# Performance work log

Hardware: AMD Instinct MI355X
Metric: run time of the kernel (lower is better)

Reference implementation:

```python
import jax, jax.numpy as jnp
import numpy as np

D = 1024
H = 16
HD = D // H
B = 2
T = 2048


def _rope_tables(t, hd):
    inv_freq = 1.0 / (10000.0 ** (np.arange(0, hd, 2, dtype=np.float32) / hd))
    ang = np.arange(t, dtype=np.float32)[:, None] * inv_freq[None, :]  # [T, hd/2]
    emb = np.concatenate([ang, ang], axis=-1)  # [T, hd]
    return jnp.asarray(np.cos(emb)), jnp.asarray(np.sin(emb))


def setup_inputs() -> dict:
    key = jax.random.key(0)
    kx, kq, kk, kv, ko = jax.random.split(key, 5)
    scale = 0.02
    x = jax.random.normal(kx, (B, T, D), dtype=jnp.float32)
    cos, sin = _rope_tables(T, HD)
    mask = jnp.tril(jnp.ones((T, T), dtype=jnp.int32))[None, None]  # [1,1,T,T]
    wq = jax.random.normal(kq, (D, D), dtype=jnp.float32) * scale
    wk = jax.random.normal(kk, (D, D), dtype=jnp.float32) * scale
    wv = jax.random.normal(kv, (D, D), dtype=jnp.float32) * scale
    wo = jax.random.normal(ko, (D, D), dtype=jnp.float32) * scale
    return {"x": x, "cos": cos, "sin": sin, "mask": mask,
            "wq": wq, "wk": wk, "wv": wv, "wo": wo}


def _rotate_half(t):
    t1, t2 = jnp.split(t, 2, axis=-1)
    return jnp.concatenate((-t2, t1), axis=-1)


def reference(x, cos, sin, mask, wq, wk, wv, wo):
    Bx, Tx, C = x.shape
    hd = C // H
    # nn.Linear: y = x @ W.T  -> [B,T,H,hd] -> [B,H,T,hd]
    q = (x @ wq.T).reshape(Bx, Tx, H, hd).transpose(0, 2, 1, 3)
    k = (x @ wk.T).reshape(Bx, Tx, H, hd).transpose(0, 2, 1, 3)
    v = (x @ wv.T).reshape(Bx, Tx, H, hd).transpose(0, 2, 1, 3)
    c = cos[:Tx][None, None]  # [1,1,T,hd]
    s = sin[:Tx][None, None]
    q = q * c + _rotate_half(q) * s
    k = k * c + _rotate_half(k) * s
    att = jnp.einsum('bhqd,bhkd->bhqk', q, k) * (hd ** -0.5)
    att = jnp.where(mask[:, :, :Tx, :Tx] == 0, -jnp.inf, att)
    att = jax.nn.softmax(att, axis=-1)
    out = jnp.einsum('bhqk,bhkd->bhqd', att, v)
    out = out.transpose(0, 2, 1, 3).reshape(Bx, Tx, C)
    return out @ wo.T
```

## Files before the change

kernel.cpp:

```cpp
#include <hip/hip_runtime.h>
#include <math.h>

constexpr int D  = 1024;
constexpr int H  = 16;
constexpr int HD = 64;
constexpr int B  = 2;
constexpr int T  = 2048;
constexpr int M  = B * T;

constexpr size_t XSZ = (size_t)M * D;
constexpr size_t WSZ = (size_t)D * D;

typedef float  f32x4   __attribute__((ext_vector_type(4)));
typedef float  f32x16  __attribute__((ext_vector_type(16)));
typedef __bf16 bf16x8  __attribute__((ext_vector_type(8)));
typedef __bf16 bf16x4  __attribute__((ext_vector_type(4)));
typedef unsigned u32x2 __attribute__((ext_vector_type(2)));
typedef unsigned u32x4 __attribute__((ext_vector_type(4)));

static __device__ inline f32x4 mfma16(bf16x8 a, bf16x8 b, f32x4 c) {
  return __builtin_amdgcn_mfma_f32_16x16x32_bf16(a, b, c, 0, 0, 0);
}
static __device__ inline f32x16 mfma32(bf16x8 a, bf16x8 b, f32x16 c) {
  return __builtin_amdgcn_mfma_f32_32x32x16_bf16(a, b, c, 0, 0, 0);
}
static __device__ inline unsigned cvtpk(float a, float b) {
  unsigned r;
  asm("v_cvt_pk_bf16_f32 %0, %1, %2" : "=v"(r) : "v"(a), "v"(b));
  return r;
}
static __device__ inline u32x2 plswap(unsigned a, unsigned b) {
  return __builtin_amdgcn_permlane32_swap(a, b, false, false);
}
static __device__ inline void gload16(const __bf16* g, __bf16* l) {
  __builtin_amdgcn_global_load_lds(
      (const __attribute__((address_space(1))) void*)g,
      (__attribute__((address_space(3))) void*)l, 16, 0, 0);
}

__global__ __launch_bounds__(256)
void cvt_all(const float* __restrict__ x, const float* __restrict__ wq,
             const float* __restrict__ wk, const float* __restrict__ wv,
             const float* __restrict__ wo, __bf16* __restrict__ out) {
  size_t idx = ((size_t)blockIdx.x * 256 + threadIdx.x) * 8;
  const float* src;
  if      (idx < XSZ)            src = x  + idx;
  else if (idx < XSZ + WSZ)      src = wq + (idx - XSZ);
  else if (idx < XSZ + 2 * WSZ)  src = wk + (idx - XSZ - WSZ);
  else if (idx < XSZ + 3 * WSZ)  src = wv + (idx - XSZ - 2 * WSZ);
  else                           src = wo + (idx - XSZ - 3 * WSZ);
  float4 a = *reinterpret_cast<const float4*>(src);
  float4 b = *reinterpret_cast<const float4*>(src + 4);
  bf16x8 o;
  o[0] = (__bf16)a.x; o[1] = (__bf16)a.y; o[2] = (__bf16)a.z; o[3] = (__bf16)a.w;
  o[4] = (__bf16)b.x; o[5] = (__bf16)b.y; o[6] = (__bf16)b.z; o[7] = (__bf16)b.w;
  *reinterpret_cast<bf16x8*>(out + idx) = o;
}

template<int MODE>
__global__ __launch_bounds__(256)
void gemm_mfma(const __bf16* __restrict__ A,
               const __bf16* __restrict__ W0, const __bf16* __restrict__ W1,
               const __bf16* __restrict__ W2,
               const float* __restrict__ cosT, const float* __restrict__ sinT,
               void* __restrict__ out0, void* __restrict__ out1,
               void* __restrict__ out2) {
  constexpr int BM  = (MODE == 0) ? 64 : 128;
  constexpr int NMT = BM / 32;
  __shared__ __bf16 As[BM * 64];
  __shared__ __bf16 Bs[128 * 64];

  const int tid  = threadIdx.x;
  const int lane = tid & 63;
  const int w    = tid >> 6;
  const int wm   = w >> 1;
  const int wn   = w & 1;
  const int l15  = lane & 15, lg = lane >> 4;
  const int m0   = blockIdx.y * BM;

  int which, n0;
  const __bf16* Bw;
  if (MODE == 1) {
    which = blockIdx.x >> 3;
    n0 = (blockIdx.x & 7) * 128;
    Bw = which == 0 ? W0 : which == 1 ? W1 : W2;
  } else {
    which = 0;
    n0 = blockIdx.x * 128;
    Bw = W0;
  }

  f32x4 acc[NMT][4];
  #pragma unroll
  for (int i = 0; i < NMT; ++i)
    #pragma unroll
    for (int j = 0; j < 4; ++j) acc[i][j] = (f32x4){0.f, 0.f, 0.f, 0.f};

  const int r0 = tid >> 3;
  const int c0 = (tid & 7) * 8;

  for (int k0 = 0; k0 < 1024; k0 += 64) {
    #pragma unroll
    for (int i = 0; i < BM / 32; ++i)
      gload16(A + (size_t)(m0 + r0 + 32 * i) * 1024 + k0 + c0,
              As + (tid + 256 * i) * 8);
    #pragma unroll
    for (int i = 0; i < 4; ++i)
      gload16(Bw + (size_t)(n0 + r0 + 32 * i) * 1024 + k0 + c0,
              Bs + (tid + 256 * i) * 8);
    __syncthreads();

    #pragma unroll
    for (int ks = 0; ks < 2; ++ks) {
      bf16x8 af[NMT], bfr[4];
      #pragma unroll
      for (int mt = 0; mt < NMT; ++mt)
        af[mt] = *reinterpret_cast<const bf16x8*>(
            &As[(wm * (BM / 2) + mt * 16 + l15) * 64 + ks * 32 + lg * 8]);
      #pragma unroll
      for (int nt = 0; nt < 4; ++nt)
        bfr[nt] = *reinterpret_cast<const bf16x8*>(
            &Bs[(wn * 64 + nt * 16 + l15) * 64 + ks * 32 + lg * 8]);
      #pragma unroll
      for (int mt = 0; mt < NMT; ++mt)
        #pragma unroll
        for (int nt = 0; nt < 4; ++nt)
          acc[mt][nt] = mfma16(af[mt], bfr[nt], acc[mt][nt]);
    }
    __syncthreads();
  }

  if (MODE == 0) {
    float* o = (float*)out0;
    #pragma unroll
    for (int mt = 0; mt < NMT; ++mt) {
      const int mb = m0 + wm * (BM / 2) + mt * 16 + lg * 4;
      #pragma unroll
      for (int nt = 0; nt < 4; ++nt) {
        const int n = n0 + wn * 64 + nt * 16 + l15;
        #pragma unroll
        for (int r = 0; r < 4; ++r)
          o[(size_t)(mb + r) * 1024 + n] = acc[mt][nt][r];
      }
    }
  } else if (which < 2) {
    __bf16* dst = which == 0 ? (__bf16*)out0 : (__bf16*)out1;
    const float qs = (which == 0) ? 0.180336880f : 1.0f;
    const int h = (n0 + wn * 64) >> 6;
    const int e  = l15 & 7;
    const int Lh = (l15 >> 3) << 5;
    #pragma unroll
    for (int mt = 0; mt < NMT; ++mt) {
      const int tb   = m0 + wm * (BM / 2) + mt * 16 + lg * 4;
      const int bb   = tb >> 11;
      const int tloc = tb & 2047;
      const int bh   = bb * H + h;
      #pragma unroll
      for (int r = 0; r < 4; ++r) {
        const int t = tloc + r;
        const int L = (t & 31) + Lh;
        size_t fb;
        if (which == 0)
          fb = ((size_t)bh * 64 + (t >> 5)) * 4;
        else
          fb = (((size_t)bh * 32 + (t >> 6)) * 2 + ((t >> 5) & 1)) * 4;
        #pragma unroll
        for (int nt = 0; nt < 2; ++nt) {
          const int hd = nt * 16 + l15;
          const float c = cosT[t * HD + hd];
          const float s = sinT[t * HD + hd];
          const float v1 = acc[mt][nt][r];
          const float v2 = acc[mt][nt + 2][r];
          dst[(fb + nt)     * 512 + L * 8 + e] = (__bf16)((v1 * c - v2 * s) * qs);
          dst[(fb + nt + 2) * 512 + L * 8 + e] = (__bf16)((v2 * c + v1 * s) * qs);
        }
      }
    }
  } else {
    __bf16* dst = (__bf16*)out2;
    const int h = (n0 + wn * 64) >> 6;
    #pragma unroll
    for (int mt = 0; mt < NMT; ++mt) {
      const int tb   = m0 + wm * (BM / 2) + mt * 16 + lg * 4;
      const int bb   = tb >> 11;
      const int tloc = tb & 2047;
      const int bh   = bb * H + h;
      const int jt   = tloc >> 6;
      const int kt   = tloc & 63;
      const int Lk   = ((kt >> 3) & 1) << 5;
      const int e0   = kt & 7;
      const size_t fb = (((size_t)bh * 32 + jt) * 2) * 4 + (kt >> 4);
      #pragma unroll
      for (int nt = 0; nt < 4; ++nt) {
        const int hd = nt * 16 + l15;
        const int dg = hd >> 5;
        const int L  = (hd & 31) + Lk;
        bf16x4 ov;
        #pragma unroll
        for (int r = 0; r < 4; ++r) ov[r] = (__bf16)acc[mt][nt][r];
        *reinterpret_cast<bf16x4*>(
            &dst[(fb + (size_t)dg * 4) * 512 + L * 8 + e0]) = ov;
      }
    }
  }
}

__global__ __launch_bounds__(256, 2)
void attn_v14(const __bf16* __restrict__ Qf, const __bf16* __restrict__ Kf,
              const __bf16* __restrict__ Vf, __bf16* __restrict__ Ob) {
  const int tid  = threadIdx.x;
  const int lane = tid & 63;
  const int w    = tid >> 6;
  const int l31  = lane & 31;
  const int hi   = lane >> 5;
  const int bx   = blockIdx.x;
  const int by   = blockIdx.y;
  const int bh   = (bx & 7) + 8 * (by >> 3);
  const int x    = (bx >> 3) + 2 * (by & 7);

  const int wi = (bh < 16) ? w : (w ^ 1);
  const int qt = (wi == 0) ? 2 * x : (wi == 1) ? 63 - 2 * x
               : (wi == 2) ? 2 * x + 1 : 62 - 2 * x;
  const int q0w = qt * 32;
  const int NT  = (qt >> 1) + 1;

  const __bf16* qbase = Qf + (((size_t)bh * 64 + qt) * 4) * 512 + lane * 8;
  bf16x8 qfr[4];
  #pragma unroll
  for (int st = 0; st < 4; ++st)
    qfr[st] = *reinterpret_cast<const bf16x8*>(qbase + st * 512);

  f32x16 zv;
  #pragma unroll
  for (int i = 0; i < 16; ++i) zv[i] = 0.f;

  float m_run = -INFINITY, l_run = 0.f;
  f32x16 oacc0, oacc1;
  #pragma unroll
  for (int i = 0; i < 16; ++i) { oacc0[i] = 0.f; oacc1[i] = 0.f; }

  const __bf16* kbase = Kf + ((size_t)bh * 32 * 8) * 512 + lane * 8;
  const __bf16* vbase = Vf + ((size_t)bh * 32 * 8) * 512 + lane * 8;

#define LOADK8(K0, K1, K2, K3, K4, K5, K6, K7, jj)                            \
  do {                                                                        \
    const __bf16* _kp = kbase + (size_t)(jj) * 8 * 512;                       \
    K0 = *reinterpret_cast<const bf16x8*>(_kp);                               \
    K1 = *reinterpret_cast<const bf16x8*>(_kp + 512);                         \
    K2 = *reinterpret_cast<const bf16x8*>(_kp + 1024);                        \
    K3 = *reinterpret_cast<const bf16x8*>(_kp + 1536);                        \
    K4 = *reinterpret_cast<const bf16x8*>(_kp + 2048);                        \
    K5 = *reinterpret_cast<const bf16x8*>(_kp + 2560);                        \
    K6 = *reinterpret_cast<const bf16x8*>(_kp + 3072);                        \
    K7 = *reinterpret_cast<const bf16x8*>(_kp + 3584);                        \
    __builtin_amdgcn_sched_barrier(0);        \
  } while (0)

#define TILE64(K0, K1, K2, K3, K4, K5, K6, K7, jj)                            \
  do {                                                                        \
            \
    const __bf16* _vp = vbase + (size_t)(jj) * 8 * 512;                       \
    bf16x8 Va00 = *reinterpret_cast<const bf16x8*>(_vp);                      \
    bf16x8 Va01 = *reinterpret_cast<const bf16x8*>(_vp + 512);                \
    bf16x8 Vb00 = *reinterpret_cast<const bf16x8*>(_vp + 1024);               \
    bf16x8 Vb01 = *reinterpret_cast<const bf16x8*>(_vp + 1536);               \
    bf16x8 Va10 = *reinterpret_cast<const bf16x8*>(_vp + 2048);               \
    bf16x8 Va11 = *reinterpret_cast<const bf16x8*>(_vp + 2560);               \
    bf16x8 Vb10 = *reinterpret_cast<const bf16x8*>(_vp + 3072);               \
    bf16x8 Vb11 = *reinterpret_cast<const bf16x8*>(_vp + 3584);               \
    __builtin_amdgcn_sched_barrier(0);                                        \
               \
    f32x16 s0a = mfma32(K0, qfr[0], zv);                                      \
    f32x16 s0b = mfma32(K1, qfr[1], zv);                                      \
    f32x16 s1a = mfma32(K4, qfr[0], zv);                                      \
    f32x16 s1b = mfma32(K5, qfr[1], zv);                                      \
    s0a = mfma32(K2, qfr[2], s0a);                                            \
    s0b = mfma32(K3, qfr[3], s0b);                                            \
    s1a = mfma32(K6, qfr[2], s1a);                                            \
    s1b = mfma32(K7, qfr[3], s1b);                                            \
    f32x16 sv0, sv1;                                                          \
    _Pragma("unroll")                                                         \
    for (int _i = 0; _i < 16; ++_i) {                                         \
      sv0[_i] = s0a[_i] + s0b[_i];                                            \
      sv1[_i] = s1a[_i] + s1b[_i];                                            \
    }                                                                         \
    if ((jj) == NT - 1) {         \
      const int _q  = q0w + l31;                                              \
      const int _k0 = (jj) * 64 + 4 * hi;                                     \
      _Pragma("unroll")                                                       \
      for (int _r = 0; _r < 16; ++_r) {                                       \
        const int _key = _k0 + (_r & 3) + 8 * (_r >> 2);                      \
        if (_key > _q)      sv0[_r] = -INFINITY;                              \
        if (_key + 32 > _q) sv1[_r] = -INFINITY;                              \
      }                                                                       \
    }                                                                         \
                                             \
    float _mx[16];                                                            \
    _Pragma("unroll")                                                         \
    for (int _i = 0; _i < 16; ++_i) _mx[_i] = fmaxf(sv0[_i], sv1[_i]);        \
    _Pragma("unroll")                                                         \
    for (int _s = 8; _s > 0; _s >>= 1)                                        \
      _Pragma("unroll")                                                       \
      for (int _i = 0; _i < 8; ++_i)                                          \
        if (_i < _s) _mx[_i] = fmaxf(_mx[_i], _mx[_i + _s]);                  \
    union { float f; unsigned u; } _cv; _cv.f = _mx[0];                       \
    u32x2 _sw = plswap(_cv.u, _cv.u);                                         \
    union { unsigned u; float f; } _c0, _c1; _c0.u = _sw[0]; _c1.u = _sw[1];  \
    const float _pmax = fmaxf(_c0.f, _c1.f);                                  \
    if (__any(_pmax > m_run + 8.f)) {                                         \
      const float _mn = fmaxf(m_run, _pmax);                                  \
      const float _rs = exp2f(m_run - _mn);                                   \
      l_run *= _rs;                                                           \
      _Pragma("unroll")                                                       \
      for (int _i = 0; _i < 16; ++_i) { oacc0[_i] *= _rs; oacc1[_i] *= _rs; } \
      m_run = _mn;                                                            \
    }                                                                         \
    _Pragma("unroll")                                                         \
    for (int _i = 0; _i < 16; ++_i) {                                         \
      sv0[_i] = exp2f(sv0[_i] - m_run);                                       \
      sv1[_i] = exp2f(sv1[_i] - m_run);                                       \
    }                                                                         \
    float _sm[16];                                                            \
    _Pragma("unroll")                                                         \
    for (int _i = 0; _i < 16; ++_i) _sm[_i] = sv0[_i] + sv1[_i];              \
    _Pragma("unroll")                                                         \
    for (int _s = 8; _s > 0; _s >>= 1)                                        \
      _Pragma("unroll")                                                       \
      for (int _i = 0; _i < 8; ++_i)                                          \
        if (_i < _s) _sm[_i] += _sm[_i + _s];                                 \
    l_run += _sm[0];                                                          \
    unsigned _cp0[8], _cp1[8];                                                \
    _Pragma("unroll")                                                         \
    for (int _m = 0; _m < 4; ++_m) {                                          \
      _cp0[2 * _m]     = cvtpk(sv0[4 * _m],     sv0[4 * _m + 1]);             \
      _cp0[2 * _m + 1] = cvtpk(sv0[4 * _m + 2], sv0[4 * _m + 3]);             \
      _cp1[2 * _m]     = cvtpk(sv1[4 * _m],     sv1[4 * _m + 1]);             \
      _cp1[2 * _m + 1] = cvtpk(sv1[4 * _m + 2], sv1[4 * _m + 3]);             \
    }                                                                         \
    {                                                                         \
      u32x2 _r0 = plswap(_cp0[0], _cp0[2]);                                   \
      u32x2 _r1 = plswap(_cp0[1], _cp0[3]);                                   \
      union { u32x4 u; bf16x8 v; } _pu;                                       \
      _pu.u = (u32x4){_r0[0], _r1[0], _r0[1], _r1[1]};                        \
      oacc0 = mfma32(Va00, _pu.v, oacc0);                                     \
      oacc1 = mfma32(Va10, _pu.v, oacc1);                                     \
    }                                                                         \
    {                                                                         \
      u32x2 _r0 = plswap(_cp0[4], _cp0[6]);                                   \
      u32x2 _r1 = plswap(_cp0[5], _cp0[7]);                                   \
      union { u32x4 u; bf16x8 v; } _pu;                                       \
      _pu.u = (u32x4){_r0[0], _r1[0], _r0[1], _r1[1]};                        \
      oacc0 = mfma32(Va01, _pu.v, oacc0);                                     \
      oacc1 = mfma32(Va11, _pu.v, oacc1);                                     \
    }                                                                         \
    {                                                                         \
      u32x2 _r0 = plswap(_cp1[0], _cp1[2]);                                   \
      u32x2 _r1 = plswap(_cp1[1], _cp1[3]);                                   \
      union { u32x4 u; bf16x8 v; } _pu;                                       \
      _pu.u = (u32x4){_r0[0], _r1[0], _r0[1], _r1[1]};                        \
      oacc0 = mfma32(Vb00, _pu.v, oacc0);                                     \
      oacc1 = mfma32(Vb10, _pu.v, oacc1);                                     \
    }                                                                         \
    {                                                                         \
      u32x2 _r0 = plswap(_cp1[4], _cp1[6]);                                   \
      u32x2 _r1 = plswap(_cp1[5], _cp1[7]);                                   \
      union { u32x4 u; bf16x8 v; } _pu;                                       \
      _pu.u = (u32x4){_r0[0], _r1[0], _r0[1], _r1[1]};                        \
      oacc0 = mfma32(Vb01, _pu.v, oacc0);                                     \
      oacc1 = mfma32(Vb11, _pu.v, oacc1);                                     \
    }                                                                         \
  } while (0)

  bf16x8 kA0, kA1, kA2, kA3, kA4, kA5, kA6, kA7;
  bf16x8 kB0, kB1, kB2, kB3, kB4, kB5, kB6, kB7;

  LOADK8(kA0, kA1, kA2, kA3, kA4, kA5, kA6, kA7, 0);
  int j = 0;
  #pragma unroll 1
  for (;;) {
    if (j + 1 < NT) LOADK8(kB0, kB1, kB2, kB3, kB4, kB5, kB6, kB7, j + 1);
    TILE64(kA0, kA1, kA2, kA3, kA4, kA5, kA6, kA7, j);
    if (++j >= NT) break;
    if (j + 1 < NT) LOADK8(kA0, kA1, kA2, kA3, kA4, kA5, kA6, kA7, j + 1);
    TILE64(kB0, kB1, kB2, kB3, kB4, kB5, kB6, kB7, j);
    if (++j >= NT) break;
  }
#undef TILE64
#undef LOADK8

  const float l_tot = l_run + __shfl_xor(l_run, 32);
  const float inv = 1.f / l_tot;
  const int b = bh >> 4, h = bh & 15;
  const int q_abs = q0w + l31;
  const size_t rowbase = ((size_t)(b * T + q_abs)) * 1024 + h * 64;
  #pragma unroll
  for (int rg = 0; rg < 4; ++rg) {
    bf16x4 o0, o1;
    #pragma unroll
    for (int r = 0; r < 4; ++r) {
      o0[r] = (__bf16)(oacc0[rg * 4 + r] * inv);
      o1[r] = (__bf16)(oacc1[rg * 4 + r] * inv);
    }
    *reinterpret_cast<bf16x4*>(&Ob[rowbase + rg * 8 + hi * 4])      = o0;
    *reinterpret_cast<bf16x4*>(&Ob[rowbase + 32 + rg * 8 + hi * 4]) = o1;
  }
}

extern "C" void kernel_launch(void* const* d_in, const int* in_sizes, int n_in,
                              void* d_out, int out_size, void* d_ws, size_t ws_size,
                              hipStream_t stream) {
  const float* x    = (const float*)d_in[0];
  const float* cosT = (const float*)d_in[1];
  const float* sinT = (const float*)d_in[2];
  const float* wq   = (const float*)d_in[4];
  const float* wk   = (const float*)d_in[5];
  const float* wv   = (const float*)d_in[6];
  const float* wo   = (const float*)d_in[7];
  float* out = (float*)d_out;

  __bf16* xb   = (__bf16*)d_ws;
  __bf16* wqb  = xb  + XSZ;
  __bf16* wkb  = wqb + WSZ;
  __bf16* wvb  = wkb + WSZ;
  __bf16* wob  = wvb + WSZ;
  __bf16* Qfb  = wob + WSZ;
  __bf16* Kfb  = Qfb + XSZ;
  __bf16* Vfb  = Kfb + XSZ;
  __bf16* attb = Vfb + XSZ;

  cvt_all<<<(XSZ + 4 * WSZ) / 8 / 256, 256, 0, stream>>>(x, wq, wk, wv, wo, xb);

  gemm_mfma<1><<<dim3(24, 32), 256, 0, stream>>>(
      xb, wqb, wkb, wvb, cosT, sinT, Qfb, Kfb, Vfb);

  attn_v14<<<dim3(16, 32), 256, 0, stream>>>(Qfb, Kfb, Vfb, attb);

  gemm_mfma<0><<<dim3(8, 64), 256, 0, stream>>>(
      attb, wob, nullptr, nullptr, nullptr, nullptr, out, nullptr, nullptr);
}
```

Measured before the change: 143.5 us.

## Software-pipeline QK^T one tile ahead of softmax and PV in attention

Splits the attention inner tile into separate QK, softmax+PV, and V-load stages, then computes the next tile's QK^T MFMAs before the current tile's softmax so matrix work overlaps the VALU-heavy softmax. K loads are prefetched two tiles ahead. The QK accumulation also changes from two parallel partial sums to one serial chain. This raises register pressure (extra score accumulators) under the 2-waves launch bound, with a risk of spills or lower occupancy.

```diff
diff --git a/kernel.cpp b/kernel.cpp
--- a/kernel.cpp
+++ b/kernel.cpp
@@ -206,7 +206,7 @@
 }
 
 __global__ __launch_bounds__(256, 2)
-void attn_v14(const __bf16* __restrict__ Qf, const __bf16* __restrict__ Kf,
+void attn_v15(const __bf16* __restrict__ Qf, const __bf16* __restrict__ Kf,
               const __bf16* __restrict__ Vf, __bf16* __restrict__ Ob) {
   const int tid  = threadIdx.x;
   const int lane = tid & 63;
@@ -253,51 +253,50 @@
     K5 = *reinterpret_cast<const bf16x8*>(_kp + 2560);                        \
     K6 = *reinterpret_cast<const bf16x8*>(_kp + 3072);                        \
     K7 = *reinterpret_cast<const bf16x8*>(_kp + 3584);                        \
-    __builtin_amdgcn_sched_barrier(0);        \
+    __builtin_amdgcn_sched_barrier(0);                                        \
   } while (0)
 
-#define TILE64(K0, K1, K2, K3, K4, K5, K6, K7, jj)                            \
+#define LOADV8(jj)                                                            \
   do {                                                                        \
-            \
     const __bf16* _vp = vbase + (size_t)(jj) * 8 * 512;                       \
-    bf16x8 Va00 = *reinterpret_cast<const bf16x8*>(_vp);                      \
-    bf16x8 Va01 = *reinterpret_cast<const bf16x8*>(_vp + 512);                \
-    bf16x8 Vb00 = *reinterpret_cast<const bf16x8*>(_vp + 1024);               \
-    bf16x8 Vb01 = *reinterpret_cast<const bf16x8*>(_vp + 1536);               \
-    bf16x8 Va10 = *reinterpret_cast<const bf16x8*>(_vp + 2048);               \
-    bf16x8 Va11 = *reinterpret_cast<const bf16x8*>(_vp + 2560);               \
-    bf16x8 Vb10 = *reinterpret_cast<const bf16x8*>(_vp + 3072);               \
-    bf16x8 Vb11 = *reinterpret_cast<const bf16x8*>(_vp + 3584);               \
+    VV0 = *reinterpret_cast<const bf16x8*>(_vp);                              \
+    VV1 = *reinterpret_cast<const bf16x8*>(_vp + 512);                        \
+    VV2 = *reinterpret_cast<const bf16x8*>(_vp + 1024);                       \
+    VV3 = *reinterpret_cast<const bf16x8*>(_vp + 1536);                       \
+    VV4 = *reinterpret_cast<const bf16x8*>(_vp + 2048);                       \
+    VV5 = *reinterpret_cast<const bf16x8*>(_vp + 2560);                       \
+    VV6 = *reinterpret_cast<const bf16x8*>(_vp + 3072);                       \
+    VV7 = *reinterpret_cast<const bf16x8*>(_vp + 3584);                       \
     __builtin_amdgcn_sched_barrier(0);                                        \
-               \
-    f32x16 s0a = mfma32(K0, qfr[0], zv);                                      \
-    f32x16 s0b = mfma32(K1, qfr[1], zv);                                      \
-    f32x16 s1a = mfma32(K4, qfr[0], zv);                                      \
-    f32x16 s1b = mfma32(K5, qfr[1], zv);                                      \
-    s0a = mfma32(K2, qfr[2], s0a);                                            \
-    s0b = mfma32(K3, qfr[3], s0b);                                            \
-    s1a = mfma32(K6, qfr[2], s1a);                                            \
-    s1b = mfma32(K7, qfr[3], s1b);                                            \
-    f32x16 sv0, sv1;                                                          \
-    _Pragma("unroll")                                                         \
-    for (int _i = 0; _i < 16; ++_i) {                                         \
-      sv0[_i] = s0a[_i] + s0b[_i];                                            \
-      sv1[_i] = s1a[_i] + s1b[_i];                                            \
-    }                                                                         \
+  } while (0)
+
+#define QK64(SV0, SV1, K0, K1, K2, K3, K4, K5, K6, K7)                        \
+  do {                                                                        \
+    SV0 = mfma32(K0, qfr[0], zv);                                             \
+    SV0 = mfma32(K1, qfr[1], SV0);                                            \
+    SV0 = mfma32(K2, qfr[2], SV0);                                            \
+    SV0 = mfma32(K3, qfr[3], SV0);                                            \
+    SV1 = mfma32(K4, qfr[0], zv);                                             \
+    SV1 = mfma32(K5, qfr[1], SV1);                                            \
+    SV1 = mfma32(K6, qfr[2], SV1);                                            \
+    SV1 = mfma32(K7, qfr[3], SV1);                                            \
+  } while (0)
+
+#define SMPV(SV0, SV1, jj)                                                    \
+  do {                                                                        \
     if ((jj) == NT - 1) {         \
       const int _q  = q0w + l31;                                              \
       const int _k0 = (jj) * 64 + 4 * hi;                                     \
       _Pragma("unroll")                                                       \
       for (int _r = 0; _r < 16; ++_r) {                                       \
         const int _key = _k0 + (_r & 3) + 8 * (_r >> 2);                      \
-        if (_key > _q)      sv0[_r] = -INFINITY;                              \
-        if (_key + 32 > _q) sv1[_r] = -INFINITY;                              \
+        if (_key > _q)      SV0[_r] = -INFINITY;                              \
+        if (_key + 32 > _q) SV1[_r] = -INFINITY;                              \
       }                                                                       \
     }                                                                         \
-                                             \
     float _mx[16];                                                            \
     _Pragma("unroll")                                                         \
-    for (int _i = 0; _i < 16; ++_i) _mx[_i] = fmaxf(sv0[_i], sv1[_i]);        \
+    for (int _i = 0; _i < 16; ++_i) _mx[_i] = fmaxf(SV0[_i], SV1[_i]);        \
     _Pragma("unroll")                                                         \
     for (int _s = 8; _s > 0; _s >>= 1)                                        \
       _Pragma("unroll")                                                       \
@@ -317,12 +316,12 @@
     }                                                                         \
     _Pragma("unroll")                                                         \
     for (int _i = 0; _i < 16; ++_i) {                                         \
-      sv0[_i] = exp2f(sv0[_i] - m_run);                                       \
-      sv1[_i] = exp2f(sv1[_i] - m_run);                                       \
+      SV0[_i] = exp2f(SV0[_i] - m_run);                                       \
+      SV1[_i] = exp2f(SV1[_i] - m_run);                                       \
     }                                                                         \
     float _sm[16];                                                            \
     _Pragma("unroll")                                                         \
-    for (int _i = 0; _i < 16; ++_i) _sm[_i] = sv0[_i] + sv1[_i];              \
+    for (int _i = 0; _i < 16; ++_i) _sm[_i] = SV0[_i] + SV1[_i];              \
     _Pragma("unroll")                                                         \
     for (int _s = 8; _s > 0; _s >>= 1)                                        \
       _Pragma("unroll")                                                       \
@@ -332,60 +331,76 @@
     unsigned _cp0[8], _cp1[8];                                                \
     _Pragma("unroll")                                                         \
     for (int _m = 0; _m < 4; ++_m) {                                          \
-      _cp0[2 * _m]     = cvtpk(sv0[4 * _m],     sv0[4 * _m + 1]);             \
-      _cp0[2 * _m + 1] = cvtpk(sv0[4 * _m + 2], sv0[4 * _m + 3]);             \
-      _cp1[2 * _m]     = cvtpk(sv1[4 * _m],     sv1[4 * _m + 1]);             \
-      _cp1[2 * _m + 1] = cvtpk(sv1[4 * _m + 2], sv1[4 * _m + 3]);             \
+      _cp0[2 * _m]     = cvtpk(SV0[4 * _m],     SV0[4 * _m + 1]);             \
+      _cp0[2 * _m + 1] = cvtpk(SV0[4 * _m + 2], SV0[4 * _m + 3]);             \
+      _cp1[2 * _m]     = cvtpk(SV1[4 * _m],     SV1[4 * _m + 1]);             \
+      _cp1[2 * _m + 1] = cvtpk(SV1[4 * _m + 2], SV1[4 * _m + 3]);             \
     }                                                                         \
     {                                                                         \
       u32x2 _r0 = plswap(_cp0[0], _cp0[2]);                                   \
       u32x2 _r1 = plswap(_cp0[1], _cp0[3]);                                   \
       union { u32x4 u; bf16x8 v; } _pu;                                       \
       _pu.u = (u32x4){_r0[0], _r1[0], _r0[1], _r1[1]};                        \
-      oacc0 = mfma32(Va00, _pu.v, oacc0);                                     \
-      oacc1 = mfma32(Va10, _pu.v, oacc1);                                     \
+      oacc0 = mfma32(VV0, _pu.v, oacc0);                                      \
+      oacc1 = mfma32(VV4, _pu.v, oacc1);                                      \
     }                                                                         \
     {                                                                         \
       u32x2 _r0 = plswap(_cp0[4], _cp0[6]);                                   \
       u32x2 _r1 = plswap(_cp0[5], _cp0[7]);                                   \
       union { u32x4 u; bf16x8 v; } _pu;                                       \
       _pu.u = (u32x4){_r0[0], _r1[0], _r0[1], _r1[1]};                        \
-      oacc0 = mfma32(Va01, _pu.v, oacc0);                                     \
-      oacc1 = mfma32(Va11, _pu.v, oacc1);                                     \
+      oacc0 = mfma32(VV1, _pu.v, oacc0);                                      \
+      oacc1 = mfma32(VV5, _pu.v, oacc1);                                      \
     }                                                                         \
     {                                                                         \
       u32x2 _r0 = plswap(_cp1[0], _cp1[2]);                                   \
       u32x2 _r1 = plswap(_cp1[1], _cp1[3]);                                   \
       union { u32x4 u; bf16x8 v; } _pu;                                       \
       _pu.u = (u32x4){_r0[0], _r1[0], _r0[1], _r1[1]};                        \
-      oacc0 = mfma32(Vb00, _pu.v, oacc0);                                     \
-      oacc1 = mfma32(Vb10, _pu.v, oacc1);                                     \
+      oacc0 = mfma32(VV2, _pu.v, oacc0);                                      \
+      oacc1 = mfma32(VV6, _pu.v, oacc1);                                      \
     }                                                                         \
     {                                                                         \
       u32x2 _r0 = plswap(_cp1[4], _cp1[6]);                                   \
       u32x2 _r1 = plswap(_cp1[5], _cp1[7]);                                   \
       union { u32x4 u; bf16x8 v; } _pu;                                       \
       _pu.u = (u32x4){_r0[0], _r1[0], _r0[1], _r1[1]};                        \
-      oacc0 = mfma32(Vb01, _pu.v, oacc0);                                     \
-      oacc1 = mfma32(Vb11, _pu.v, oacc1);                                     \
+      oacc0 = mfma32(VV3, _pu.v, oacc0);                                      \
+      oacc1 = mfma32(VV7, _pu.v, oacc1);                                      \
     }                                                                         \
   } while (0)
 
   bf16x8 kA0, kA1, kA2, kA3, kA4, kA5, kA6, kA7;
   bf16x8 kB0, kB1, kB2, kB3, kB4, kB5, kB6, kB7;
+  bf16x8 VV0, VV1, VV2, VV3, VV4, VV5, VV6, VV7;
+  f32x16 svA0, svA1, svB0, svB1;
 
   LOADK8(kA0, kA1, kA2, kA3, kA4, kA5, kA6, kA7, 0);
+  QK64(svA0, svA1, kA0, kA1, kA2, kA3, kA4, kA5, kA6, kA7);
+  if (1 < NT) LOADK8(kB0, kB1, kB2, kB3, kB4, kB5, kB6, kB7, 1);
+
   int j = 0;
   #pragma unroll 1
   for (;;) {
-    if (j + 1 < NT) LOADK8(kB0, kB1, kB2, kB3, kB4, kB5, kB6, kB7, j + 1);
-    TILE64(kA0, kA1, kA2, kA3, kA4, kA5, kA6, kA7, j);
+    LOADV8(j);
+    if (j + 1 < NT)
+      QK64(svB0, svB1, kB0, kB1, kB2, kB3, kB4, kB5, kB6, kB7);
+    if (j + 2 < NT)
+      LOADK8(kA0, kA1, kA2, kA3, kA4, kA5, kA6, kA7, j + 2);
+    SMPV(svA0, svA1, j);
     if (++j >= NT) break;
-    if (j + 1 < NT) LOADK8(kA0, kA1, kA2, kA3, kA4, kA5, kA6, kA7, j + 1);
-    TILE64(kB0, kB1, kB2, kB3, kB4, kB5, kB6, kB7, j);
+
+    LOADV8(j);
+    if (j + 1 < NT)
+      QK64(svA0, svA1, kA0, kA1, kA2, kA3, kA4, kA5, kA6, kA7);
+    if (j + 2 < NT)
+      LOADK8(kB0, kB1, kB2, kB3, kB4, kB5, kB6, kB7, j + 2);
+    SMPV(svB0, svB1, j);
     if (++j >= NT) break;
   }
-#undef TILE64
+#undef SMPV
+#undef QK64
+#undef LOADV8
 #undef LOADK8
 
   const float l_tot = l_run + __shfl_xor(l_run, 32);
@@ -433,7 +448,7 @@
   gemm_mfma<1><<<dim3(24, 32), 256, 0, stream>>>(
       xb, wqb, wkb, wvb, cosT, sinT, Qfb, Kfb, Vfb);
 
-  attn_v14<<<dim3(16, 32), 256, 0, stream>>>(Qfb, Kfb, Vfb, attb);
+  attn_v15<<<dim3(16, 32), 256, 0, stream>>>(Qfb, Kfb, Vfb, attb);
 
   gemm_mfma<0><<<dim3(8, 64), 256, 0, stream>>>(
       attb, wob, nullptr, nullptr, nullptr, nullptr, out, nullptr, nullptr);
```

New measurement: 141.3 us. No clear change (-1.6%).
